# Kernel optimization log

Measured on AMD Instinct MI355X. Metric: run time of the kernel, lower is better.

Reference implementation:

```python
import jax, jax.numpy as jnp
import numpy as np

HIDDEN = 1024
N_HEADS = 16
N_LAYERS = 10
LOCAL_K = 3
TOKEN_T, TOKEN_H, TOKEN_W = 4, 16, 16
PATCH_SIZE = 2
LATENT_C = 16
TOKEN_DIM = LATENT_C * PATCH_SIZE * PATCH_SIZE  # 64
TOKEN_IN = TOKEN_DIM + 1                        # 65
N_TOKENS = TOKEN_T * TOKEN_H * TOKEN_W          # 1024
B = 1
HEAD_DIM = HIDDEN // N_HEADS
LN_EPS = 1e-5


def layer_norm(x, w, b):
    m = x.mean(-1, keepdims=True)
    v = ((x - m) ** 2).mean(-1, keepdims=True)
    return (x - m) * jax.lax.rsqrt(v + LN_EPS) * w + b


def patchify(lat):
    Bx, T, C, H, W = lat.shape
    ph, pw = H // PATCH_SIZE, W // PATCH_SIZE
    x = lat.reshape(Bx, T, C, ph, PATCH_SIZE, pw, PATCH_SIZE)
    x = x.transpose(0, 1, 3, 5, 2, 4, 6)
    return x.reshape(Bx, T * ph * pw, C * PATCH_SIZE * PATCH_SIZE)


def unpatchify(tok):
    Bx = tok.shape[0]
    C = TOKEN_DIM // (PATCH_SIZE * PATCH_SIZE)
    x = tok.reshape(Bx, TOKEN_T, TOKEN_H, TOKEN_W, C, PATCH_SIZE, PATCH_SIZE)
    x = x.transpose(0, 1, 4, 2, 5, 3, 6)
    return x.reshape(Bx, TOKEN_T, C, TOKEN_H * PATCH_SIZE, TOKEN_W * PATCH_SIZE)


def gather_neighbors(kv):
    # kv: (B, N, 2D) -> (B, N, 27, 2D), 3x3x3 zero-padded neighborhoods
    Bx, Nx, D2 = kv.shape
    pad = LOCAL_K // 2
    x = kv.reshape(Bx, TOKEN_T, TOKEN_H, TOKEN_W, D2)
    x = jnp.pad(x, ((0, 0), (pad, pad), (pad, pad), (pad, pad), (0, 0)))
    sl = [x[:, dt:dt + TOKEN_T, dh:dh + TOKEN_H, dw:dw + TOKEN_W]
          for dt in range(LOCAL_K) for dh in range(LOCAL_K) for dw in range(LOCAL_K)]
    nb = jnp.stack(sl, axis=4)  # (B,T,H,W,27,2D)
    return nb.reshape(Bx, Nx, LOCAL_K ** 3, D2)


def local_attention(x, qkv_w, out_w):
    Bx, Nx, D = x.shape
    H, d = N_HEADS, HEAD_DIM
    qkv = x @ qkv_w                       # (B,N,3D)
    q, k, v = jnp.split(qkv, 3, axis=-1)
    kv_nb = gather_neighbors(jnp.concatenate([k, v], axis=-1))  # (B,N,27,2D)
    k_nb, v_nb = jnp.split(kv_nb, 2, axis=-1)
    q = q.reshape(Bx, Nx, H, d)
    k_nb = k_nb.reshape(Bx, Nx, LOCAL_K ** 3, H, d)
    v_nb = v_nb.reshape(Bx, Nx, LOCAL_K ** 3, H, d)
    scores = jnp.einsum('bnhd,bnkhd->bnhk', q, k_nb) / np.sqrt(d).astype(np.float32)
    probs = jax.nn.softmax(scores, axis=-1)
    out = jnp.einsum('bnhk,bnkhd->bnhd', probs, v_nb).reshape(Bx, Nx, D)
    return out @ out_w


def global_attention(x, mask_flat, qkv_w, out_w):
    # Each masked query attends to all N keys; math identical to the
    # gather/SDPA/scatter in the original (per-query attention is independent),
    # realized as full attention masked to zero at unmasked positions.
    Bx, Nx, D = x.shape
    H, d = N_HEADS, HEAD_DIM
    qkv = x @ qkv_w
    q, k, v = jnp.split(qkv, 3, axis=-1)
    q = q.reshape(Bx, Nx, H, d)
    k = k.reshape(Bx, Nx, H, d)
    v = v.reshape(Bx, Nx, H, d)
    scores = jnp.einsum('bqhd,bkhd->bhqk', q, k) / np.sqrt(d).astype(np.float32)
    probs = jax.nn.softmax(scores, axis=-1)
    out = jnp.einsum('bhqk,bkhd->bqhd', probs, v).reshape(Bx, Nx, D)
    out = out @ out_w
    return out * mask_flat[..., None].astype(out.dtype)


def setup_inputs() -> dict:
    key = jax.random.key(0)
    ks = jax.random.split(key, 24)
    s = 0.02
    L, D = N_LAYERS, HIDDEN
    inp = {
        'latents': jax.random.normal(ks[0], (B, TOKEN_T, LATENT_C, TOKEN_H * PATCH_SIZE, TOKEN_W * PATCH_SIZE), jnp.float32),
        'token_mask': jax.random.uniform(ks[1], (B, TOKEN_T, TOKEN_H, TOKEN_W)) < 0.1,
        'input_proj_w': jax.random.normal(ks[2], (TOKEN_IN, D), jnp.float32) * s,
        'input_proj_b': jnp.zeros((D,), jnp.float32),
        'emb_t': jax.random.normal(ks[3], (TOKEN_T, D), jnp.float32) * s,
        'emb_h': jax.random.normal(ks[4], (TOKEN_H, D), jnp.float32) * s,
        'emb_w': jax.random.normal(ks[5], (TOKEN_W, D), jnp.float32) * s,
        'ln_local_w': jnp.ones((L, D), jnp.float32),
        'ln_local_b': jnp.zeros((L, D), jnp.float32),
        'ln_global_w': jnp.ones((L, D), jnp.float32),
        'ln_global_b': jnp.zeros((L, D), jnp.float32),
        'ln_ffn_w': jnp.ones((L, D), jnp.float32),
        'ln_ffn_b': jnp.zeros((L, D), jnp.float32),
        'local_qkv_w': jax.random.normal(ks[6], (L, D, 3 * D), jnp.float32) * s,
        'local_out_w': jax.random.normal(ks[7], (L, D, D), jnp.float32) * s,
        'global_qkv_w': jax.random.normal(ks[8], (L, D, 3 * D), jnp.float32) * s,
        'global_out_w': jax.random.normal(ks[9], (L, D, D), jnp.float32) * s,
        'ffn_w1': jax.random.normal(ks[10], (L, D, 4 * D), jnp.float32) * s,
        'ffn_b1': jnp.zeros((L, 4 * D), jnp.float32),
        'ffn_w2': jax.random.normal(ks[11], (L, 4 * D, D), jnp.float32) * s,
        'ffn_b2': jnp.zeros((L, D), jnp.float32),
        'final_ln_w': jnp.ones((D,), jnp.float32),
        'final_ln_b': jnp.zeros((D,), jnp.float32),
        # original zero-inits output_proj; use small random so the test is non-trivial
        'out_proj_w': jax.random.normal(ks[12], (D, TOKEN_DIM), jnp.float32) * s,
        'out_proj_b': jnp.zeros((TOKEN_DIM,), jnp.float32),
    }
    return inp


def reference(latents, token_mask, input_proj_w, input_proj_b, emb_t, emb_h, emb_w,
              ln_local_w, ln_local_b, ln_global_w, ln_global_b, ln_ffn_w, ln_ffn_b,
              local_qkv_w, local_out_w, global_qkv_w, global_out_w,
              ffn_w1, ffn_b1, ffn_w2, ffn_b2, final_ln_w, final_ln_b,
              out_proj_w, out_proj_b):
    Bx = latents.shape[0]
    mask_flat = token_mask.reshape(Bx, -1)
    tokens = patchify(latents)                       # (B, N, TOKEN_DIM)
    flag = mask_flat[..., None].astype(tokens.dtype)
    x = jnp.concatenate([tokens, flag], axis=-1) @ input_proj_w + input_proj_b

    tt, hh, ww = jnp.meshgrid(jnp.arange(TOKEN_T), jnp.arange(TOKEN_H), jnp.arange(TOKEN_W), indexing='ij')
    pos = emb_t[tt.reshape(-1)] + emb_h[hh.reshape(-1)] + emb_w[ww.reshape(-1)]
    x = x + pos[None]

    for l in range(N_LAYERS):
        x = x + local_attention(layer_norm(x, ln_local_w[l], ln_local_b[l]), local_qkv_w[l], local_out_w[l])
        x = x + global_attention(layer_norm(x, ln_global_w[l], ln_global_b[l]), mask_flat, global_qkv_w[l], global_out_w[l])
        h = layer_norm(x, ln_ffn_w[l], ln_ffn_b[l])
        h = jax.nn.gelu(h @ ffn_w1[l] + ffn_b1[l], approximate=False) @ ffn_w2[l] + ffn_b2[l]
        x = x + h

    delta = layer_norm(x, final_ln_w, final_ln_b) @ out_proj_w + out_proj_b
    return unpatchify(tokens + delta)
```

## Files before the change

kernel.cpp:

```cpp
#include <hip/hip_runtime.h>
#include <hip/hip_bf16.h>
#include <math.h>

typedef __bf16 bf16;
typedef __bf16 bf16x8 __attribute__((ext_vector_type(8)));
typedef __bf16 bf16x4 __attribute__((ext_vector_type(4)));
typedef float  f32x4 __attribute__((ext_vector_type(4)));
typedef unsigned int u32x4 __attribute__((ext_vector_type(4)));

#define NTOK 1024
#define HID  1024
#define NH   16
#define HD   64
#define NL   10
#define QCMAX 256

#define EPI_F32  0
#define EPI_GELU 1

__global__ __launch_bounds__(256)
void wtrans_k(const float* __restrict__ W, bf16* __restrict__ Wt, int K, int N)
{
    __shared__ bf16 tile[64][72];
    const long mofs = (long)blockIdx.z * K * N;
    const float* Ws = W + mofs;
    bf16* Wo = Wt + mofs;
    const int n0 = blockIdx.x * 64, k0 = blockIdx.y * 64;
    const int t = threadIdx.x;
    {
        const int r = t >> 2, cc = (t & 3) * 16;
        const float* src = Ws + (long)(k0 + r) * N + n0 + cc;
#pragma unroll
        for (int i = 0; i < 2; ++i) {
            f32x4 a = *(const f32x4*)(src + i * 8);
            f32x4 b = *(const f32x4*)(src + i * 8 + 4);
            bf16x8 w;
            w[0]=(bf16)a.x; w[1]=(bf16)a.y; w[2]=(bf16)a.z; w[3]=(bf16)a.w;
            w[4]=(bf16)b.x; w[5]=(bf16)b.y; w[6]=(bf16)b.z; w[7]=(bf16)b.w;
            *(bf16x8*)&tile[r][cc + i * 8] = w;
        }
    }
    __syncthreads();
    {
        const int n = t >> 2, kc = (t & 3) * 16;
        bf16x8 o0, o1;
#pragma unroll
        for (int j = 0; j < 8; ++j) { o0[j] = tile[kc + j][n]; o1[j] = tile[kc + 8 + j][n]; }
        bf16* dst = Wo + (long)(n0 + n) * K + k0 + kc;
        *(bf16x8*)dst = o0;
        *(bf16x8*)(dst + 8) = o1;
    }
}

template<int EPI, int BM, int BN, int KSPLIT>
__global__ __launch_bounds__(256)
void gemm_k(const bf16* __restrict__ A, int lda, long bsA,
            const bf16* __restrict__ Bt, int ldb, long bsB,
            void* __restrict__ Cv, int ldc, long bsC,
            const float* __restrict__ bias, int K)
{
    constexpr int WC  = (BM == 128) ? 2 : 4;
    constexpr int WTN = BN / WC;
    constexpr int NF  = WTN / 16;
    __shared__ bf16 Al[2][BM * 32];
    __shared__ bf16 Bl[2][BN * 32];

    const int t    = threadIdx.x;
    const int lane = t & 63;
    const int wv   = t >> 6;
    const int wr   = wv / WC, wc = wv % WC;
    const int lrow = lane & 15, lk = lane >> 4;
    const int n0   = blockIdx.x * BN;
    const int m0   = blockIdx.y * BM;
    const int ks   = (KSPLIT > 1) ? (blockIdx.z % KSPLIT) : 0;
    const int bz   = (KSPLIT > 1) ? (blockIdx.z / KSPLIT) : blockIdx.z;
    const int Kc   = K / KSPLIT;

    const bf16* Ab = A  + bsA * bz + (long)ks * Kc;
    const bf16* Bb = Bt + bsB * bz + (long)ks * Kc;

    f32x4 acc[4][NF];
#pragma unroll
    for (int m = 0; m < 4; ++m)
#pragma unroll
        for (int n = 0; n < NF; ++n) acc[m][n] = f32x4{0.f, 0.f, 0.f, 0.f};

    const int sr = t >> 2, sc = (t & 3) * 8;

    auto stage = [&](int buf, int kk) {
#pragma unroll
        for (int i = 0; i < BM / 64; ++i)
            __builtin_amdgcn_global_load_lds(
                (const __attribute__((address_space(1))) void*)(Ab + (long)(m0 + sr + i * 64) * lda + kk + sc),
                (__attribute__((address_space(3))) void*)(&Al[buf][i * 2048 + t * 8]), 16, 0, 0);
#pragma unroll
        for (int i = 0; i < BN / 64; ++i)
            __builtin_amdgcn_global_load_lds(
                (const __attribute__((address_space(1))) void*)(Bb + (long)(n0 + sr + i * 64) * ldb + kk + sc),
                (__attribute__((address_space(3))) void*)(&Bl[buf][i * 2048 + t * 8]), 16, 0, 0);
    };

    stage(0, 0);
    __syncthreads();
    int cur = 0;
    for (int k0 = 0; k0 < Kc; k0 += 32) {
        if (k0 + 32 < Kc) stage(cur ^ 1, k0 + 32);
        bf16x8 af[4], bfv[NF];
#pragma unroll
        for (int m = 0; m < 4; ++m)
            af[m] = *(const bf16x8*)&Al[cur][(wr * 64 + m * 16 + lrow) * 32 + lk * 8];
#pragma unroll
        for (int n = 0; n < NF; ++n)
            bfv[n] = *(const bf16x8*)&Bl[cur][(wc * WTN + n * 16 + lrow) * 32 + lk * 8];
#pragma unroll
        for (int m = 0; m < 4; ++m)
#pragma unroll
            for (int n = 0; n < NF; ++n)
                acc[m][n] = __builtin_amdgcn_mfma_f32_16x16x32_bf16(af[m], bfv[n], acc[m][n], 0, 0, 0);
        __syncthreads();
        cur ^= 1;
    }

    float* Cf = (float*)Cv + bsC * blockIdx.z;
    bf16*  Cb = (bf16*)Cv + bsC * blockIdx.z;
#pragma unroll
    for (int m = 0; m < 4; ++m)
#pragma unroll
        for (int n = 0; n < NF; ++n) {
            const int c = n0 + wc * WTN + n * 16 + lrow;
#pragma unroll
            for (int q = 0; q < 4; ++q) {
                const int r = m0 + wr * 64 + m * 16 + lk * 4 + q;
                const float v = acc[m][n][q];
                const long off = (long)r * ldc + c;
                if (EPI == EPI_F32) Cf[off] = v;
                else {
                    float u = v + bias[c];
                    Cb[off] = (bf16)(0.5f * u * (1.f + erff(u * 0.70710678118654752f)));
                }
            }
        }
}

template<int NS, bool BIAS, bool SCATTER>
__global__ __launch_bounds__(256)
void ln_add_k(float* __restrict__ x, const float* __restrict__ parts, long pstride,
              const float* __restrict__ bias, const int* __restrict__ rmap,
              const float* __restrict__ w, const float* __restrict__ b,
              bf16* __restrict__ o)
{
    int row  = blockIdx.x * 4 + (threadIdx.x >> 6);
    int lane = threadIdx.x & 63;
    f32x4* xr = (f32x4*)(x + (long)row * HID) + lane * 4;
    f32x4 v[4];
#pragma unroll
    for (int i = 0; i < 4; ++i) v[i] = xr[i];

    if (NS > 0) {
        int prow = SCATTER ? rmap[row] : row;
        if (!SCATTER || prow >= 0) {
            const float* pp = parts + (long)prow * 1024 + lane * 16;
#pragma unroll
            for (int ksi = 0; ksi < NS; ++ksi) {
                const f32x4* q = (const f32x4*)(pp + (long)ksi * pstride);
#pragma unroll
                for (int i = 0; i < 4; ++i) v[i] += q[i];
            }
            if (BIAS) {
                const f32x4* bb = (const f32x4*)bias + lane * 4;
#pragma unroll
                for (int i = 0; i < 4; ++i) v[i] += bb[i];
            }
#pragma unroll
            for (int i = 0; i < 4; ++i) xr[i] = v[i];
        }
    }

    float s = 0.f;
#pragma unroll
    for (int i = 0; i < 4; ++i) s += v[i].x + v[i].y + v[i].z + v[i].w;
    for (int m = 32; m; m >>= 1) s += __shfl_xor(s, m);
    float mean = s * (1.f / 1024.f);
    f32x4 d[4];
    float ss = 0.f;
#pragma unroll
    for (int i = 0; i < 4; ++i) {
        d[i] = v[i] - mean;
        ss += d[i].x * d[i].x + d[i].y * d[i].y + d[i].z * d[i].z + d[i].w * d[i].w;
    }
    for (int m = 32; m; m >>= 1) ss += __shfl_xor(ss, m);
    float rs = rsqrtf(ss * (1.f / 1024.f) + 1e-5f);
    const f32x4* wp = (const f32x4*)w + lane * 4;
    const f32x4* bp = (const f32x4*)b + lane * 4;
    bf16x8 o0, o1;
#pragma unroll
    for (int i = 0; i < 4; ++i) {
        f32x4 wv = wp[i], bv = bp[i];
        f32x4 e;
        e.x = d[i].x * rs * wv.x + bv.x; e.y = d[i].y * rs * wv.y + bv.y;
        e.z = d[i].z * rs * wv.z + bv.z; e.w = d[i].w * rs * wv.w + bv.w;
        if (i < 2) { o0[i*4+0]=(bf16)e.x; o0[i*4+1]=(bf16)e.y; o0[i*4+2]=(bf16)e.z; o0[i*4+3]=(bf16)e.w; }
        else       { int k=(i-2)*4; o1[k+0]=(bf16)e.x; o1[k+1]=(bf16)e.y; o1[k+2]=(bf16)e.z; o1[k+3]=(bf16)e.w; }
    }
    bf16* op = o + (long)row * HID + lane * 16;
    *(bf16x8*)op = o0;
    *(bf16x8*)(op + 8) = o1;
}

__global__ __launch_bounds__(256)
void red4pv_k(const float* __restrict__ p, bf16* __restrict__ Oc)
{
    int i = blockIdx.x * 256 + threadIdx.x;
    int d4 = (i & 15) * 4;
    int r  = (i >> 4) & 255;
    int h  = i >> 12;
    const float* base = p + (long)(h * 4) * 16384 + r * 64 + d4;
    f32x4 s = *(const f32x4*)base;
    s += *(const f32x4*)(base + 16384);
    s += *(const f32x4*)(base + 32768);
    s += *(const f32x4*)(base + 49152);
    bf16x4 o;
    o[0] = (bf16)s.x; o[1] = (bf16)s.y; o[2] = (bf16)s.z; o[3] = (bf16)s.w;
    *(bf16x4*)(Oc + (long)r * 1024 + h * 64 + d4) = o;
}

__global__ __launch_bounds__(256)
void lattn_k(const float* __restrict__ qkv, bf16* __restrict__ ao)
{
    int w    = blockIdx.x * 4 + (threadIdx.x >> 6);
    int lane = threadIdx.x & 63;
    int n = w >> 4, h = w & 15;
    int tt = n >> 8, hh = (n >> 4) & 15, ww = n & 15;

    int nj = -1;
    float dotv = 0.f;
    if (lane < 27) {
        int dt = lane / 9 - 1, dh = (lane % 9) / 3 - 1, dw = lane % 3 - 1;
        int t2 = tt + dt, h2 = hh + dh, w2 = ww + dw;
        if (t2 >= 0 && t2 < 4 && h2 >= 0 && h2 < 16 && w2 >= 0 && w2 < 16)
            nj = (t2 << 8) | (h2 << 4) | w2;
    }
    if (nj >= 0) {
        const f32x4* qp = (const f32x4*)(qkv + (long)n * 3072 + h * 64);
        const f32x4* kp = (const f32x4*)(qkv + (long)nj * 3072 + 1024 + h * 64);
#pragma unroll
        for (int i = 0; i < 16; ++i) {
            f32x4 q4 = qp[i], k4 = kp[i];
            dotv += q4.x * k4.x + q4.y * k4.y + q4.z * k4.z + q4.w * k4.w;
        }
    }
    float sc = (lane < 27) ? dotv * 0.125f : -3.0e38f;
    float mx = sc;
    for (int m = 32; m; m >>= 1) mx = fmaxf(mx, __shfl_xor(mx, m));
    float e = (lane < 27) ? __expf(sc - mx) : 0.f;
    float s = e;
    for (int m = 32; m; m >>= 1) s += __shfl_xor(s, m);
    float p = e / s;

    float acc = 0.f;
    for (int j = 0; j < 27; ++j) {
        float pj = __shfl(p, j);
        int  njj = __shfl(nj, j);
        if (njj >= 0) acc += pj * qkv[(long)njj * 3072 + 2048 + h * 64 + lane];
    }
    ao[(long)n * 1024 + h * 64 + lane] = (bf16)acc;
}

__global__ void compact_k(const int* __restrict__ mask, int* __restrict__ qidx,
                          int* __restrict__ rmap)
{
    int lane = threadIdx.x;
    int total = 0;
    for (int base = 0; base < 1024; base += 64) {
        int m = (mask[base + lane] != 0) ? 1 : 0;
        unsigned long long bal = __ballot(m);
        int pos = total + (int)__popcll(bal & ((1ull << lane) - 1ull));
        int ok = (m && pos < QCMAX);
        if (ok) qidx[pos] = base + lane;
        rmap[base + lane] = ok ? pos : -1;
        total += (int)__popcll(bal);
    }
    for (int i = total + lane; i < QCMAX; i += 64) qidx[i] = -1;
}

__global__ __launch_bounds__(256)
void qkvbuild_k(const float* __restrict__ qkv, const int* __restrict__ qidx,
                bf16* __restrict__ Qc, bf16* __restrict__ Kh, bf16* __restrict__ Vt)
{
    __shared__ bf16 vt[64][72];
    const int h = blockIdx.y;
    const int t = threadIdx.x;
    if (blockIdx.x < 4) {
        const int r = blockIdx.x * 64 + (t >> 2), dc = (t & 3) * 16;
        const int q = qidx[r];
        bf16x8 o0, o1;
        if (q >= 0) {
            const f32x4* src = (const f32x4*)(qkv + (long)q * 3072 + h * 64 + dc);
#pragma unroll
            for (int i = 0; i < 2; ++i) {
                f32x4 a = src[i * 2] * 0.125f, b = src[i * 2 + 1] * 0.125f;
                bf16x8 w;
                w[0]=(bf16)a.x; w[1]=(bf16)a.y; w[2]=(bf16)a.z; w[3]=(bf16)a.w;
                w[4]=(bf16)b.x; w[5]=(bf16)b.y; w[6]=(bf16)b.z; w[7]=(bf16)b.w;
                if (i == 0) o0 = w; else o1 = w;
            }
        } else {
#pragma unroll
            for (int j = 0; j < 8; ++j) { o0[j] = (bf16)0.f; o1[j] = (bf16)0.f; }
        }
        bf16* dst = Qc + (long)h * (QCMAX * 64) + (long)r * 64 + dc;
        *(bf16x8*)dst = o0;
        *(bf16x8*)(dst + 8) = o1;
        return;
    }
    const int k0 = (blockIdx.x - 4) * 64;
    {
        const int r = t >> 2, dc = (t & 3) * 16;
        const float* kp = qkv + (long)(k0 + r) * 3072 + 1024 + h * 64 + dc;
        const float* vp = kp + 1024;
        bf16x8 ko0, ko1;
#pragma unroll
        for (int i = 0; i < 2; ++i) {
            f32x4 a = *(const f32x4*)(kp + i * 8);
            f32x4 b = *(const f32x4*)(kp + i * 8 + 4);
            bf16x8 w;
            w[0]=(bf16)a.x; w[1]=(bf16)a.y; w[2]=(bf16)a.z; w[3]=(bf16)a.w;
            w[4]=(bf16)b.x; w[5]=(bf16)b.y; w[6]=(bf16)b.z; w[7]=(bf16)b.w;
            if (i == 0) ko0 = w; else ko1 = w;
        }
        bf16* kd = Kh + (long)h * (NTOK * 64) + (long)(k0 + r) * 64 + dc;
        *(bf16x8*)kd = ko0;
        *(bf16x8*)(kd + 8) = ko1;
#pragma unroll
        for (int i = 0; i < 2; ++i) {
            f32x4 a = *(const f32x4*)(vp + i * 8);
            f32x4 b = *(const f32x4*)(vp + i * 8 + 4);
            bf16x8 w;
            w[0]=(bf16)a.x; w[1]=(bf16)a.y; w[2]=(bf16)a.z; w[3]=(bf16)a.w;
            w[4]=(bf16)b.x; w[5]=(bf16)b.y; w[6]=(bf16)b.z; w[7]=(bf16)b.w;
            *(bf16x8*)&vt[r][dc + i * 8] = w;
        }
    }
    __syncthreads();
    {
        const int d = t >> 2, kc = (t & 3) * 16;
        bf16x8 o0, o1;
#pragma unroll
        for (int j = 0; j < 8; ++j) { o0[j] = vt[kc + j][d]; o1[j] = vt[kc + 8 + j][d]; }
        bf16* dst = Vt + (long)h * (64 * NTOK) + (long)d * NTOK + k0 + kc;
        *(bf16x8*)dst = o0;
        *(bf16x8*)(dst + 8) = o1;
    }
}

__global__ __launch_bounds__(256)
void softmax_k(const float* __restrict__ S, bf16* __restrict__ P)
{
    int row  = blockIdx.x * 4 + (threadIdx.x >> 6);
    int lane = threadIdx.x & 63;
    const f32x4* sp = (const f32x4*)(S + (long)row * 1024) + lane * 4;
    f32x4 v[4];
#pragma unroll
    for (int i = 0; i < 4; ++i) v[i] = sp[i];
    float mx = -3.0e38f;
#pragma unroll
    for (int i = 0; i < 4; ++i)
        mx = fmaxf(mx, fmaxf(fmaxf(v[i].x, v[i].y), fmaxf(v[i].z, v[i].w)));
    for (int m = 32; m; m >>= 1) mx = fmaxf(mx, __shfl_xor(mx, m));
    f32x4 ev[4];
    float sum = 0.f;
#pragma unroll
    for (int i = 0; i < 4; ++i) {
        ev[i].x = __expf(v[i].x - mx); ev[i].y = __expf(v[i].y - mx);
        ev[i].z = __expf(v[i].z - mx); ev[i].w = __expf(v[i].w - mx);
        sum += ev[i].x + ev[i].y + ev[i].z + ev[i].w;
    }
    for (int m = 32; m; m >>= 1) sum += __shfl_xor(sum, m);
    float inv = 1.f / sum;
    bf16x8 o0, o1;
#pragma unroll
    for (int i = 0; i < 4; ++i) {
        f32x4 e = ev[i] * inv;
        if (i < 2) { o0[i*4+0]=(bf16)e.x; o0[i*4+1]=(bf16)e.y; o0[i*4+2]=(bf16)e.z; o0[i*4+3]=(bf16)e.w; }
        else       { int k=(i-2)*4; o1[k+0]=(bf16)e.x; o1[k+1]=(bf16)e.y; o1[k+2]=(bf16)e.z; o1[k+3]=(bf16)e.w; }
    }
    bf16* op = P + (long)row * 1024 + lane * 16;
    *(bf16x8*)op = o0;
    *(bf16x8*)(op + 8) = o1;
}

__global__ __launch_bounds__(256)
void prep_k(const float* __restrict__ lat, const int* __restrict__ mask,
            const float* __restrict__ Wi, const float* __restrict__ bi,
            const float* __restrict__ et, const float* __restrict__ eh,
            const float* __restrict__ ew,
            float* __restrict__ x, float* __restrict__ tokens)
{
    __shared__ float tl[16][65];
    int t = threadIdx.x;
    int n0 = blockIdx.x * 16;
    for (int idx = t; idx < 16 * 65; idx += 256) {
        int ti = idx / 65, d = idx % 65;
        int n = n0 + ti;
        int tt = n >> 8, hh = (n >> 4) & 15, wwi = n & 15;
        float v;
        if (d < 64) {
            int c = d >> 2, ph = (d >> 1) & 1, pw = d & 1;
            v = lat[(((long)tt * 16 + c) * 32 + hh * 2 + ph) * 32 + wwi * 2 + pw];
            tokens[(long)n * 64 + d] = v;
        } else {
            v = mask[n] ? 1.f : 0.f;
        }
        tl[ti][d] = v;
    }
    __syncthreads();
    f32x4 acc[16];
#pragma unroll
    for (int i = 0; i < 16; ++i) acc[i] = f32x4{0.f, 0.f, 0.f, 0.f};
    for (int d = 0; d < 65; ++d) {
        f32x4 wv = *(const f32x4*)(Wi + (long)d * 1024 + t * 4);
#pragma unroll
        for (int ti = 0; ti < 16; ++ti) acc[ti] += tl[ti][d] * wv;
    }
    f32x4 bb = *(const f32x4*)(bi + t * 4);
    for (int ti = 0; ti < 16; ++ti) {
        int n = n0 + ti;
        int tt = n >> 8, hh = (n >> 4) & 15, wwi = n & 15;
        f32x4 pos = *(const f32x4*)(et + (long)tt * 1024 + t * 4)
                  + *(const f32x4*)(eh + (long)hh * 1024 + t * 4)
                  + *(const f32x4*)(ew + (long)wwi * 1024 + t * 4);
        *(f32x4*)(x + (long)n * 1024 + t * 4) = acc[ti] + bb + pos;
    }
}

__global__ __launch_bounds__(256)
void final_k(const bf16* __restrict__ xn, const float* __restrict__ OW,
             const float* __restrict__ ob, const float* __restrict__ tokens,
             float* __restrict__ out)
{
    __shared__ bf16 xl[8][1024];
    __shared__ float part[4][8][64];
    int t = threadIdx.x;
    int n0 = blockIdx.x * 8;
    for (int i = t; i < 1024; i += 256)
        ((u32x4*)xl)[i] = ((const u32x4*)(xn + (long)n0 * 1024))[i];
    __syncthreads();
    int j = t & 63, s = t >> 6;
    float acc[8] = {0.f, 0.f, 0.f, 0.f, 0.f, 0.f, 0.f, 0.f};
    for (int k = s * 256; k < s * 256 + 256; ++k) {
        float w = OW[(long)k * 64 + j];
#pragma unroll
        for (int ti = 0; ti < 8; ++ti) acc[ti] += (float)xl[ti][k] * w;
    }
    for (int ti = 0; ti < 8; ++ti) part[s][ti][j] = acc[ti];
    __syncthreads();
    if (s == 0) {
        for (int ti = 0; ti < 8; ++ti) {
            int n = n0 + ti;
            float v = part[0][ti][j] + part[1][ti][j] + part[2][ti][j] + part[3][ti][j]
                    + ob[j] + tokens[(long)n * 64 + j];
            int tt = n >> 8, hh = (n >> 4) & 15, wwi = n & 15;
            int c = j >> 2, ph = (j >> 1) & 1, pw = j & 1;
            out[(((long)tt * 16 + c) * 32 + hh * 2 + ph) * 32 + wwi * 2 + pw] = v;
        }
    }
}

extern "C" void kernel_launch(void* const* d_in, const int* in_sizes, int n_in,
                              void* d_out, int out_size, void* d_ws, size_t ws_size,
                              hipStream_t stream)
{
    const float* latents = (const float*)d_in[0];
    const int*   mask    = (const int*)d_in[1];
    const float* ipw  = (const float*)d_in[2];
    const float* ipb  = (const float*)d_in[3];
    const float* et   = (const float*)d_in[4];
    const float* eh   = (const float*)d_in[5];
    const float* ew   = (const float*)d_in[6];
    const float* lnlw = (const float*)d_in[7];
    const float* lnlb = (const float*)d_in[8];
    const float* lngw = (const float*)d_in[9];
    const float* lngb = (const float*)d_in[10];
    const float* lnfw = (const float*)d_in[11];
    const float* lnfb = (const float*)d_in[12];
    const float* lqkv = (const float*)d_in[13];
    const float* lout = (const float*)d_in[14];
    const float* gqkv = (const float*)d_in[15];
    const float* gout = (const float*)d_in[16];
    const float* w1   = (const float*)d_in[17];
    const float* b1   = (const float*)d_in[18];
    const float* w2   = (const float*)d_in[19];
    const float* b2   = (const float*)d_in[20];
    const float* flw  = (const float*)d_in[21];
    const float* flb  = (const float*)d_in[22];
    const float* opw  = (const float*)d_in[23];
    const float* opb  = (const float*)d_in[24];

    char* p = (char*)d_ws;
    auto alloc = [&](size_t bytes) { char* r = p; p += (bytes + 255) & ~(size_t)255; return r; };
    float* x      = (float*)alloc((size_t)4 << 20);
    bf16*  xn     = (bf16*)alloc((size_t)2 << 20);
    float* qkv    = (float*)alloc((size_t)12 << 20);
    bf16*  ao     = (bf16*)alloc((size_t)2 << 20);
    bf16*  hbuf   = (bf16*)alloc((size_t)8 << 20);
    float* tokens = (float*)alloc((size_t)256 << 10);
    bf16*  Qc     = (bf16*)alloc((size_t)512 << 10);
    bf16*  Kh     = (bf16*)alloc((size_t)2 << 20);
    bf16*  Vt     = (bf16*)alloc((size_t)2 << 20);
    float* S      = (float*)alloc((size_t)16 << 20);
    bf16*  P      = (bf16*)alloc((size_t)8 << 20);
    bf16*  Oc     = (bf16*)alloc((size_t)512 << 10);
    int*   qidx   = (int*)alloc(4096);
    int*   rmap   = (int*)alloc(4096);
    float* loutp = (float*)alloc((size_t)2 * 1024 * 1024 * 4);
    float* goutp = (float*)alloc((size_t)8 * 256 * 1024 * 4);
    float* pvp   = (float*)alloc((size_t)64 * 256 * 64 * 4);
    float* f2p   = (float*)alloc((size_t)4 * 1024 * 1024 * 4);
    bf16* lqkvT = (bf16*)alloc((size_t)10 * 3072 * 1024 * 2);
    bf16* loutT = (bf16*)alloc((size_t)10 * 1024 * 1024 * 2);
    bf16* gqkvT = (bf16*)alloc((size_t)10 * 3072 * 1024 * 2);
    bf16* goutT = (bf16*)alloc((size_t)10 * 1024 * 1024 * 2);
    bf16* w1T   = (bf16*)alloc((size_t)10 * 4096 * 1024 * 2);
    bf16* w2T   = (bf16*)alloc((size_t)10 * 1024 * 4096 * 2);

    wtrans_k<<<dim3(48, 16, NL), 256, 0, stream>>>(lqkv, lqkvT, 1024, 3072);
    wtrans_k<<<dim3(16, 16, NL), 256, 0, stream>>>(lout, loutT, 1024, 1024);
    wtrans_k<<<dim3(48, 16, NL), 256, 0, stream>>>(gqkv, gqkvT, 1024, 3072);
    wtrans_k<<<dim3(16, 16, NL), 256, 0, stream>>>(gout, goutT, 1024, 1024);
    wtrans_k<<<dim3(64, 16, NL), 256, 0, stream>>>(w1, w1T, 1024, 4096);
    wtrans_k<<<dim3(16, 64, NL), 256, 0, stream>>>(w2, w2T, 4096, 1024);

    prep_k<<<64, 256, 0, stream>>>(latents, mask, ipw, ipb, et, eh, ew, x, tokens);
    compact_k<<<1, 64, 0, stream>>>(mask, qidx, rmap);

    for (int l = 0; l < NL; ++l) {
        const long wq  = (long)l * 3072 * 1024;
        const long wo  = (long)l * 1024 * 1024;
        const long wf1 = (long)l * 4096 * 1024;

        if (l == 0)
            ln_add_k<0, false, false><<<256, 256, 0, stream>>>(
                x, nullptr, 0, nullptr, nullptr, lnlw, lnlb, xn);
        else
            ln_add_k<4, true, false><<<256, 256, 0, stream>>>(
                x, f2p, (long)1024 * 1024, b2 + (l - 1) * 1024, nullptr,
                lnlw + l * HID, lnlb + l * HID, xn);

        gemm_k<EPI_F32, 64, 128, 1><<<dim3(24, 16, 1), 256, 0, stream>>>(
            xn, 1024, 0, lqkvT + wq, 1024, 0, qkv, 3072, 0, nullptr, 1024);
        lattn_k<<<4096, 256, 0, stream>>>(qkv, ao);
        gemm_k<EPI_F32, 64, 128, 2><<<dim3(8, 16, 2), 256, 0, stream>>>(
            ao, 1024, 0, loutT + wo, 1024, 0, loutp, 1024, (long)1024 * 1024, nullptr, 1024);

        ln_add_k<2, false, false><<<256, 256, 0, stream>>>(
            x, loutp, (long)1024 * 1024, nullptr, nullptr,
            lngw + l * HID, lngb + l * HID, xn);

        gemm_k<EPI_F32, 64, 128, 1><<<dim3(24, 16, 1), 256, 0, stream>>>(
            xn, 1024, 0, gqkvT + wq, 1024, 0, qkv, 3072, 0, nullptr, 1024);
        qkvbuild_k<<<dim3(20, 16), 256, 0, stream>>>(qkv, qidx, Qc, Kh, Vt);
        gemm_k<EPI_F32, 64, 128, 1><<<dim3(8, 4, 16), 256, 0, stream>>>(
            Qc, 64, (long)256 * 64, Kh, 64, (long)1024 * 64,
            S, 1024, (long)256 * 1024, nullptr, 64);
        softmax_k<<<1024, 256, 0, stream>>>(S, P);
        gemm_k<EPI_F32, 64, 64, 4><<<dim3(1, 4, 64), 256, 0, stream>>>(
            P, 1024, (long)256 * 1024, Vt, 1024, (long)64 * 1024,
            pvp, 64, (long)256 * 64, nullptr, 1024);
        red4pv_k<<<256, 256, 0, stream>>>(pvp, Oc);
        gemm_k<EPI_F32, 64, 128, 8><<<dim3(8, 4, 8), 256, 0, stream>>>(
            Oc, 1024, 0, goutT + wo, 1024, 0, goutp, 1024, (long)256 * 1024, nullptr, 1024);

        ln_add_k<8, false, true><<<256, 256, 0, stream>>>(
            x, goutp, (long)256 * 1024, nullptr, rmap,
            lnfw + l * HID, lnfb + l * HID, xn);

        gemm_k<EPI_GELU, 64, 128, 1><<<dim3(32, 16, 1), 256, 0, stream>>>(
            xn, 1024, 0, w1T + wf1, 1024, 0, hbuf, 4096, 0, b1 + l * 4096, 1024);
        gemm_k<EPI_F32, 64, 128, 4><<<dim3(8, 16, 4), 256, 0, stream>>>(
            hbuf, 4096, 0, w2T + wf1, 4096, 0, f2p, 1024, (long)1024 * 1024, nullptr, 4096);
    }

    ln_add_k<4, true, false><<<256, 256, 0, stream>>>(
        x, f2p, (long)1024 * 1024, b2 + 9 * 1024, nullptr, flw, flb, xn);
    final_k<<<128, 256, 0, stream>>>(xn, opw, opb, tokens, (float*)d_out);
}
```

Baseline: 2.225 ms.

## Fuse global attention into flash-style kernel, add residual GEMM epilogue, merge weight transposes

Replaces the global-attention chain (Q/K/V build, QK^T GEMM, softmax, PV GEMM, split-K reduction) with one flash-attention style kernel using online softmax and MFMA. This removes the large S and P intermediate buffers and several launches. The local-attention output GEMM now accumulates straight into x through a residual epilogue instead of writing split-K partials that a later LN pass sums. The six weight-transpose launches are merged into one. The fused attention kernel runs only 128 blocks of 128 threads and loops over K/V tiles one after another, so the GPU is lightly occupied during that step.

```diff
diff --git a/kernel.cpp b/kernel.cpp
--- a/kernel.cpp
+++ b/kernel.cpp
@@ -10,22 +10,35 @@
 
 #define NTOK 1024
 #define HID  1024
-#define NH   16
-#define HD   64
 #define NL   10
 #define QCMAX 256
 
-#define EPI_F32  0
-#define EPI_GELU 1
+#define EPI_F32   0
+#define EPI_GELU  1
+#define EPI_RESID 2
 
 __global__ __launch_bounds__(256)
-void wtrans_k(const float* __restrict__ W, bf16* __restrict__ Wt, int K, int N)
+void wtransall_k(const float* __restrict__ lqkv, const float* __restrict__ lout,
+                 const float* __restrict__ gqkv, const float* __restrict__ gout,
+                 const float* __restrict__ w1,   const float* __restrict__ w2,
+                 bf16* __restrict__ lqkvT, bf16* __restrict__ loutT,
+                 bf16* __restrict__ gqkvT, bf16* __restrict__ goutT,
+                 bf16* __restrict__ w1T,   bf16* __restrict__ w2T)
 {
     __shared__ bf16 tile[64][72];
+    const int b = blockIdx.x;
+    const float* W; bf16* O; int K, N, ti;
+    if      (b < 768)  { W = lqkv; O = lqkvT; K = 1024; N = 3072; ti = b; }
+    else if (b < 1024) { W = lout; O = loutT; K = 1024; N = 1024; ti = b - 768; }
+    else if (b < 1792) { W = gqkv; O = gqkvT; K = 1024; N = 3072; ti = b - 1024; }
+    else if (b < 2048) { W = gout; O = goutT; K = 1024; N = 1024; ti = b - 1792; }
+    else if (b < 3072) { W = w1;   O = w1T;   K = 1024; N = 4096; ti = b - 2048; }
+    else               { W = w2;   O = w2T;   K = 4096; N = 1024; ti = b - 3072; }
+    const int ntx = N >> 6;
+    const int n0 = (ti % ntx) * 64, k0 = (ti / ntx) * 64;
     const long mofs = (long)blockIdx.z * K * N;
     const float* Ws = W + mofs;
-    bf16* Wo = Wt + mofs;
-    const int n0 = blockIdx.x * 64, k0 = blockIdx.y * 64;
+    bf16* Wo = O + mofs;
     const int t = threadIdx.x;
     {
         const int r = t >> 2, cc = (t & 3) * 16;
@@ -33,10 +46,10 @@
 #pragma unroll
         for (int i = 0; i < 2; ++i) {
             f32x4 a = *(const f32x4*)(src + i * 8);
-            f32x4 b = *(const f32x4*)(src + i * 8 + 4);
+            f32x4 bb = *(const f32x4*)(src + i * 8 + 4);
             bf16x8 w;
-            w[0]=(bf16)a.x; w[1]=(bf16)a.y; w[2]=(bf16)a.z; w[3]=(bf16)a.w;
-            w[4]=(bf16)b.x; w[5]=(bf16)b.y; w[6]=(bf16)b.z; w[7]=(bf16)b.w;
+            w[0]=(bf16)a.x;  w[1]=(bf16)a.y;  w[2]=(bf16)a.z;  w[3]=(bf16)a.w;
+            w[4]=(bf16)bb.x; w[5]=(bf16)bb.y; w[6]=(bf16)bb.z; w[7]=(bf16)bb.w;
             *(bf16x8*)&tile[r][cc + i * 8] = w;
         }
     }
@@ -133,7 +146,8 @@
                 const int r = m0 + wr * 64 + m * 16 + lk * 4 + q;
                 const float v = acc[m][n][q];
                 const long off = (long)r * ldc + c;
-                if (EPI == EPI_F32) Cf[off] = v;
+                if (EPI == EPI_F32)        Cf[off] = v;
+                else if (EPI == EPI_RESID) Cf[off] += v;
                 else {
                     float u = v + bias[c];
                     Cb[off] = (bf16)(0.5f * u * (1.f + erff(u * 0.70710678118654752f)));
@@ -207,21 +221,129 @@
     *(bf16x8*)(op + 8) = o1;
 }
 
-__global__ __launch_bounds__(256)
-void red4pv_k(const float* __restrict__ p, bf16* __restrict__ Oc)
-{
-    int i = blockIdx.x * 256 + threadIdx.x;
-    int d4 = (i & 15) * 4;
-    int r  = (i >> 4) & 255;
-    int h  = i >> 12;
-    const float* base = p + (long)(h * 4) * 16384 + r * 64 + d4;
-    f32x4 s = *(const f32x4*)base;
-    s += *(const f32x4*)(base + 16384);
-    s += *(const f32x4*)(base + 32768);
-    s += *(const f32x4*)(base + 49152);
-    bf16x4 o;
-    o[0] = (bf16)s.x; o[1] = (bf16)s.y; o[2] = (bf16)s.z; o[3] = (bf16)s.w;
-    *(bf16x4*)(Oc + (long)r * 1024 + h * 64 + d4) = o;
+__global__ __launch_bounds__(128)
+void gattn_k(const float* __restrict__ qkv, const int* __restrict__ qidx,
+             bf16* __restrict__ Oc)
+{
+    __shared__ bf16 Kl[64][72];
+    __shared__ bf16 Vl[64][72];
+    __shared__ bf16 Pl[2][16][72];
+
+    const int t = threadIdx.x;
+    const int w = t >> 6, lane = t & 63;
+    const int lrow = lane & 15, lk = lane >> 4;
+    const int h = blockIdx.y;
+    const int q0 = blockIdx.x * 32 + w * 16;
+
+    bf16x8 qf[2];
+#pragma unroll
+    for (int kk = 0; kk < 2; ++kk)
+#pragma unroll
+        for (int j = 0; j < 8; ++j) qf[kk][j] = (bf16)0.f;
+    {
+        const int tok = qidx[q0 + lrow];
+        if (tok >= 0) {
+            const float* qp = qkv + (long)tok * 3072 + h * 64;
+#pragma unroll
+            for (int kk = 0; kk < 2; ++kk) {
+                f32x4 a = *(const f32x4*)(qp + kk * 32 + lk * 8);
+                f32x4 b = *(const f32x4*)(qp + kk * 32 + lk * 8 + 4);
+                qf[kk][0]=(bf16)(a.x*0.125f); qf[kk][1]=(bf16)(a.y*0.125f);
+                qf[kk][2]=(bf16)(a.z*0.125f); qf[kk][3]=(bf16)(a.w*0.125f);
+                qf[kk][4]=(bf16)(b.x*0.125f); qf[kk][5]=(bf16)(b.y*0.125f);
+                qf[kk][6]=(bf16)(b.z*0.125f); qf[kk][7]=(bf16)(b.w*0.125f);
+            }
+        }
+    }
+
+    f32x4 oacc[4];
+#pragma unroll
+    for (int nf = 0; nf < 4; ++nf) oacc[nf] = f32x4{0.f, 0.f, 0.f, 0.f};
+    float m_r[4] = {-3.0e38f, -3.0e38f, -3.0e38f, -3.0e38f};
+    float l_r[4] = {0.f, 0.f, 0.f, 0.f};
+
+    const int stok = t >> 1;
+    const int sd0  = (t & 1) * 32;
+
+    for (int kt = 0; kt < 16; ++kt) {
+        __syncthreads();
+        {
+            const float* kp = qkv + (long)(kt * 64 + stok) * 3072 + 1024 + h * 64 + sd0;
+            const float* vp = kp + 1024;
+            float kv[32], vv[32];
+#pragma unroll
+            for (int i = 0; i < 8; ++i) {
+                *(f32x4*)&kv[i * 4] = *(const f32x4*)(kp + i * 4);
+                *(f32x4*)&vv[i * 4] = *(const f32x4*)(vp + i * 4);
+            }
+            bf16* kd = &Kl[stok][sd0];
+#pragma unroll
+            for (int i = 0; i < 4; ++i) {
+                bf16x8 wv;
+#pragma unroll
+                for (int j = 0; j < 8; ++j) wv[j] = (bf16)kv[i * 8 + j];
+                *(bf16x8*)(kd + i * 8) = wv;
+            }
+#pragma unroll
+            for (int i = 0; i < 32; ++i) Vl[sd0 + i][stok] = (bf16)vv[i];
+        }
+        __syncthreads();
+
+        f32x4 s[4];
+#pragma unroll
+        for (int nf = 0; nf < 4; ++nf) {
+            bf16x8 b0 = *(const bf16x8*)&Kl[nf * 16 + lrow][lk * 8];
+            bf16x8 b1 = *(const bf16x8*)&Kl[nf * 16 + lrow][32 + lk * 8];
+            f32x4 z = f32x4{0.f, 0.f, 0.f, 0.f};
+            z = __builtin_amdgcn_mfma_f32_16x16x32_bf16(qf[0], b0, z, 0, 0, 0);
+            s[nf] = __builtin_amdgcn_mfma_f32_16x16x32_bf16(qf[1], b1, z, 0, 0, 0);
+        }
+#pragma unroll
+        for (int q = 0; q < 4; ++q) {
+            float pm = fmaxf(fmaxf(s[0][q], s[1][q]), fmaxf(s[2][q], s[3][q]));
+#pragma unroll
+            for (int msk = 1; msk < 16; msk <<= 1) pm = fmaxf(pm, __shfl_xor(pm, msk));
+            float mnew = fmaxf(m_r[q], pm);
+            float scale = __expf(m_r[q] - mnew);
+            m_r[q] = mnew;
+            float ls = 0.f;
+#pragma unroll
+            for (int nf = 0; nf < 4; ++nf) {
+                float pv = __expf(s[nf][q] - mnew);
+                s[nf][q] = pv;
+                ls += pv;
+            }
+#pragma unroll
+            for (int msk = 1; msk < 16; msk <<= 1) ls += __shfl_xor(ls, msk);
+            l_r[q] = l_r[q] * scale + ls;
+#pragma unroll
+            for (int nf = 0; nf < 4; ++nf) oacc[nf][q] *= scale;
+        }
+#pragma unroll
+        for (int nf = 0; nf < 4; ++nf)
+#pragma unroll
+            for (int q = 0; q < 4; ++q)
+                Pl[w][lk * 4 + q][nf * 16 + lrow] = (bf16)s[nf][q];
+        __syncthreads();
+#pragma unroll
+        for (int kk = 0; kk < 2; ++kk) {
+            bf16x8 pa = *(const bf16x8*)&Pl[w][lrow][kk * 32 + lk * 8];
+#pragma unroll
+            for (int nf = 0; nf < 4; ++nf) {
+                bf16x8 vb = *(const bf16x8*)&Vl[nf * 16 + lrow][kk * 32 + lk * 8];
+                oacc[nf] = __builtin_amdgcn_mfma_f32_16x16x32_bf16(pa, vb, oacc[nf], 0, 0, 0);
+            }
+        }
+    }
+
+#pragma unroll
+    for (int q = 0; q < 4; ++q) {
+        float inv = 1.f / l_r[q];
+        const int r = q0 + lk * 4 + q;
+#pragma unroll
+        for (int nf = 0; nf < 4; ++nf)
+            Oc[(long)r * 1024 + h * 64 + nf * 16 + lrow] = (bf16)(oacc[nf][q] * inv);
+    }
 }
 
 __global__ __launch_bounds__(256)
@@ -281,112 +403,6 @@
         total += (int)__popcll(bal);
     }
     for (int i = total + lane; i < QCMAX; i += 64) qidx[i] = -1;
-}
-
-__global__ __launch_bounds__(256)
-void qkvbuild_k(const float* __restrict__ qkv, const int* __restrict__ qidx,
-                bf16* __restrict__ Qc, bf16* __restrict__ Kh, bf16* __restrict__ Vt)
-{
-    __shared__ bf16 vt[64][72];
-    const int h = blockIdx.y;
-    const int t = threadIdx.x;
-    if (blockIdx.x < 4) {
-        const int r = blockIdx.x * 64 + (t >> 2), dc = (t & 3) * 16;
-        const int q = qidx[r];
-        bf16x8 o0, o1;
-        if (q >= 0) {
-            const f32x4* src = (const f32x4*)(qkv + (long)q * 3072 + h * 64 + dc);
-#pragma unroll
-            for (int i = 0; i < 2; ++i) {
-                f32x4 a = src[i * 2] * 0.125f, b = src[i * 2 + 1] * 0.125f;
-                bf16x8 w;
-                w[0]=(bf16)a.x; w[1]=(bf16)a.y; w[2]=(bf16)a.z; w[3]=(bf16)a.w;
-                w[4]=(bf16)b.x; w[5]=(bf16)b.y; w[6]=(bf16)b.z; w[7]=(bf16)b.w;
-                if (i == 0) o0 = w; else o1 = w;
-            }
-        } else {
-#pragma unroll
-            for (int j = 0; j < 8; ++j) { o0[j] = (bf16)0.f; o1[j] = (bf16)0.f; }
-        }
-        bf16* dst = Qc + (long)h * (QCMAX * 64) + (long)r * 64 + dc;
-        *(bf16x8*)dst = o0;
-        *(bf16x8*)(dst + 8) = o1;
-        return;
-    }
-    const int k0 = (blockIdx.x - 4) * 64;
-    {
-        const int r = t >> 2, dc = (t & 3) * 16;
-        const float* kp = qkv + (long)(k0 + r) * 3072 + 1024 + h * 64 + dc;
-        const float* vp = kp + 1024;
-        bf16x8 ko0, ko1;
-#pragma unroll
-        for (int i = 0; i < 2; ++i) {
-            f32x4 a = *(const f32x4*)(kp + i * 8);
-            f32x4 b = *(const f32x4*)(kp + i * 8 + 4);
-            bf16x8 w;
-            w[0]=(bf16)a.x; w[1]=(bf16)a.y; w[2]=(bf16)a.z; w[3]=(bf16)a.w;
-            w[4]=(bf16)b.x; w[5]=(bf16)b.y; w[6]=(bf16)b.z; w[7]=(bf16)b.w;
-            if (i == 0) ko0 = w; else ko1 = w;
-        }
-        bf16* kd = Kh + (long)h * (NTOK * 64) + (long)(k0 + r) * 64 + dc;
-        *(bf16x8*)kd = ko0;
-        *(bf16x8*)(kd + 8) = ko1;
-#pragma unroll
-        for (int i = 0; i < 2; ++i) {
-            f32x4 a = *(const f32x4*)(vp + i * 8);
-            f32x4 b = *(const f32x4*)(vp + i * 8 + 4);
-            bf16x8 w;
-            w[0]=(bf16)a.x; w[1]=(bf16)a.y; w[2]=(bf16)a.z; w[3]=(bf16)a.w;
-            w[4]=(bf16)b.x; w[5]=(bf16)b.y; w[6]=(bf16)b.z; w[7]=(bf16)b.w;
-            *(bf16x8*)&vt[r][dc + i * 8] = w;
-        }
-    }
-    __syncthreads();
-    {
-        const int d = t >> 2, kc = (t & 3) * 16;
-        bf16x8 o0, o1;
-#pragma unroll
-        for (int j = 0; j < 8; ++j) { o0[j] = vt[kc + j][d]; o1[j] = vt[kc + 8 + j][d]; }
-        bf16* dst = Vt + (long)h * (64 * NTOK) + (long)d * NTOK + k0 + kc;
-        *(bf16x8*)dst = o0;
-        *(bf16x8*)(dst + 8) = o1;
-    }
-}
-
-__global__ __launch_bounds__(256)
-void softmax_k(const float* __restrict__ S, bf16* __restrict__ P)
-{
-    int row  = blockIdx.x * 4 + (threadIdx.x >> 6);
-    int lane = threadIdx.x & 63;
-    const f32x4* sp = (const f32x4*)(S + (long)row * 1024) + lane * 4;
-    f32x4 v[4];
-#pragma unroll
-    for (int i = 0; i < 4; ++i) v[i] = sp[i];
-    float mx = -3.0e38f;
-#pragma unroll
-    for (int i = 0; i < 4; ++i)
-        mx = fmaxf(mx, fmaxf(fmaxf(v[i].x, v[i].y), fmaxf(v[i].z, v[i].w)));
-    for (int m = 32; m; m >>= 1) mx = fmaxf(mx, __shfl_xor(mx, m));
-    f32x4 ev[4];
-    float sum = 0.f;
-#pragma unroll
-    for (int i = 0; i < 4; ++i) {
-        ev[i].x = __expf(v[i].x - mx); ev[i].y = __expf(v[i].y - mx);
-        ev[i].z = __expf(v[i].z - mx); ev[i].w = __expf(v[i].w - mx);
-        sum += ev[i].x + ev[i].y + ev[i].z + ev[i].w;
-    }
-    for (int m = 32; m; m >>= 1) sum += __shfl_xor(sum, m);
-    float inv = 1.f / sum;
-    bf16x8 o0, o1;
-#pragma unroll
-    for (int i = 0; i < 4; ++i) {
-        f32x4 e = ev[i] * inv;
-        if (i < 2) { o0[i*4+0]=(bf16)e.x; o0[i*4+1]=(bf16)e.y; o0[i*4+2]=(bf16)e.z; o0[i*4+3]=(bf16)e.w; }
-        else       { int k=(i-2)*4; o1[k+0]=(bf16)e.x; o1[k+1]=(bf16)e.y; o1[k+2]=(bf16)e.z; o1[k+3]=(bf16)e.w; }
-    }
-    bf16* op = P + (long)row * 1024 + lane * 16;
-    *(bf16x8*)op = o0;
-    *(bf16x8*)(op + 8) = o1;
 }
 
 __global__ __launch_bounds__(256)
@@ -504,18 +520,11 @@
     bf16*  ao     = (bf16*)alloc((size_t)2 << 20);
     bf16*  hbuf   = (bf16*)alloc((size_t)8 << 20);
     float* tokens = (float*)alloc((size_t)256 << 10);
-    bf16*  Qc     = (bf16*)alloc((size_t)512 << 10);
-    bf16*  Kh     = (bf16*)alloc((size_t)2 << 20);
-    bf16*  Vt     = (bf16*)alloc((size_t)2 << 20);
-    float* S      = (float*)alloc((size_t)16 << 20);
-    bf16*  P      = (bf16*)alloc((size_t)8 << 20);
     bf16*  Oc     = (bf16*)alloc((size_t)512 << 10);
     int*   qidx   = (int*)alloc(4096);
     int*   rmap   = (int*)alloc(4096);
-    float* loutp = (float*)alloc((size_t)2 * 1024 * 1024 * 4);
-    float* goutp = (float*)alloc((size_t)8 * 256 * 1024 * 4);
-    float* pvp   = (float*)alloc((size_t)64 * 256 * 64 * 4);
-    float* f2p   = (float*)alloc((size_t)4 * 1024 * 1024 * 4);
+    float* goutp  = (float*)alloc((size_t)8 * 256 * 1024 * 4);
+    float* f2p    = (float*)alloc((size_t)4 * 1024 * 1024 * 4);
     bf16* lqkvT = (bf16*)alloc((size_t)10 * 3072 * 1024 * 2);
     bf16* loutT = (bf16*)alloc((size_t)10 * 1024 * 1024 * 2);
     bf16* gqkvT = (bf16*)alloc((size_t)10 * 3072 * 1024 * 2);
@@ -523,12 +532,8 @@
     bf16* w1T   = (bf16*)alloc((size_t)10 * 4096 * 1024 * 2);
     bf16* w2T   = (bf16*)alloc((size_t)10 * 1024 * 4096 * 2);
 
-    wtrans_k<<<dim3(48, 16, NL), 256, 0, stream>>>(lqkv, lqkvT, 1024, 3072);
-    wtrans_k<<<dim3(16, 16, NL), 256, 0, stream>>>(lout, loutT, 1024, 1024);
-    wtrans_k<<<dim3(48, 16, NL), 256, 0, stream>>>(gqkv, gqkvT, 1024, 3072);
-    wtrans_k<<<dim3(16, 16, NL), 256, 0, stream>>>(gout, goutT, 1024, 1024);
-    wtrans_k<<<dim3(64, 16, NL), 256, 0, stream>>>(w1, w1T, 1024, 4096);
-    wtrans_k<<<dim3(16, 64, NL), 256, 0, stream>>>(w2, w2T, 4096, 1024);
+    wtransall_k<<<dim3(4096, 1, NL), 256, 0, stream>>>(
+        lqkv, lout, gqkv, gout, w1, w2, lqkvT, loutT, gqkvT, goutT, w1T, w2T);
 
     prep_k<<<64, 256, 0, stream>>>(latents, mask, ipw, ipb, et, eh, ew, x, tokens);
     compact_k<<<1, 64, 0, stream>>>(mask, qidx, rmap);
@@ -549,24 +554,15 @@
         gemm_k<EPI_F32, 64, 128, 1><<<dim3(24, 16, 1), 256, 0, stream>>>(
             xn, 1024, 0, lqkvT + wq, 1024, 0, qkv, 3072, 0, nullptr, 1024);
         lattn_k<<<4096, 256, 0, stream>>>(qkv, ao);
-        gemm_k<EPI_F32, 64, 128, 2><<<dim3(8, 16, 2), 256, 0, stream>>>(
-            ao, 1024, 0, loutT + wo, 1024, 0, loutp, 1024, (long)1024 * 1024, nullptr, 1024);
-
-        ln_add_k<2, false, false><<<256, 256, 0, stream>>>(
-            x, loutp, (long)1024 * 1024, nullptr, nullptr,
-            lngw + l * HID, lngb + l * HID, xn);
+        gemm_k<EPI_RESID, 64, 128, 1><<<dim3(8, 16, 1), 256, 0, stream>>>(
+            ao, 1024, 0, loutT + wo, 1024, 0, x, 1024, 0, nullptr, 1024);
+
+        ln_add_k<0, false, false><<<256, 256, 0, stream>>>(
+            x, nullptr, 0, nullptr, nullptr, lngw + l * HID, lngb + l * HID, xn);
 
         gemm_k<EPI_F32, 64, 128, 1><<<dim3(24, 16, 1), 256, 0, stream>>>(
             xn, 1024, 0, gqkvT + wq, 1024, 0, qkv, 3072, 0, nullptr, 1024);
-        qkvbuild_k<<<dim3(20, 16), 256, 0, stream>>>(qkv, qidx, Qc, Kh, Vt);
-        gemm_k<EPI_F32, 64, 128, 1><<<dim3(8, 4, 16), 256, 0, stream>>>(
-            Qc, 64, (long)256 * 64, Kh, 64, (long)1024 * 64,
-            S, 1024, (long)256 * 1024, nullptr, 64);
-        softmax_k<<<1024, 256, 0, stream>>>(S, P);
-        gemm_k<EPI_F32, 64, 64, 4><<<dim3(1, 4, 64), 256, 0, stream>>>(
-            P, 1024, (long)256 * 1024, Vt, 1024, (long)64 * 1024,
-            pvp, 64, (long)256 * 64, nullptr, 1024);
-        red4pv_k<<<256, 256, 0, stream>>>(pvp, Oc);
+        gattn_k<<<dim3(8, 16), 128, 0, stream>>>(qkv, qidx, Oc);
         gemm_k<EPI_F32, 64, 128, 8><<<dim3(8, 4, 8), 256, 0, stream>>>(
             Oc, 1024, 0, goutT + wo, 1024, 0, goutp, 1024, (long)256 * 1024, nullptr, 1024);
 
```

New measurement: 2.514 ms. 1.13x slower.
